# Optimization experiments

Hardware: AMD Instinct MI355X
Metric: run time of the kernel (lower is better)

## Reference

```python
import jax, jax.numpy as jnp
import numpy as np
from jax import lax

DIM = 1024
INNER = 2048  # dim * expand_factor
STATE = 64
B, T = 4, 2048
DECAY = 0.95
INPUT_FACTOR = 0.05
LN_EPS = 1e-5


def setup_inputs() -> dict:
    key = jax.random.key(0)
    ks = jax.random.split(key, 8)
    s = 0.02  # small weight scale
    return {
        "x": jax.random.normal(ks[0], (B, T, DIM), jnp.float32),
        "W_in": jax.random.normal(ks[1], (2 * INNER, DIM), jnp.float32) * s,
        "conv_w": jax.random.normal(ks[2], (INNER, 1, 4), jnp.float32) * s,
        "conv_b": jax.random.normal(ks[3], (INNER,), jnp.float32) * s,
        "W_B": jax.random.normal(ks[4], (STATE, INNER), jnp.float32) * s,
        "W_C": jax.random.normal(ks[5], (INNER, STATE), jnp.float32) * s,
        "D_param": jax.random.normal(ks[6], (INNER,), jnp.float32) * s,
        "W_out": jax.random.normal(ks[7], (DIM, INNER), jnp.float32) * s,
        "ln_gamma": jnp.ones((DIM,), jnp.float32),
        "ln_beta": jnp.zeros((DIM,), jnp.float32),
    }


def _layernorm(x, g, b):
    mu = jnp.mean(x, axis=-1, keepdims=True)
    var = jnp.mean(jnp.square(x - mu), axis=-1, keepdims=True)
    return (x - mu) * lax.rsqrt(var + LN_EPS) * g + b


def reference(x, W_in, conv_w, conv_b, W_B, W_C, D_param, W_out, ln_gamma, ln_beta):
    Bn, Tn, Dn = x.shape
    # in_proj -> split into input/gate halves
    x_proj = jnp.einsum("btd,ed->bte", x, W_in)  # [B,T,2*INNER]
    x_input, x_gate = jnp.split(x_proj, 2, axis=-1)
    # depthwise causal conv1d (torch pad=3 then slice [:T] == left-pad 3)
    xc = lax.conv_general_dilated(
        x_input.transpose(0, 2, 1),  # [B,C,T]
        conv_w,                       # [C,1,4]
        window_strides=(1,),
        padding=[(3, 0)],
        feature_group_count=INNER,
    ) + conv_b[None, :, None]
    u = jax.nn.silu(xc).transpose(0, 2, 1)  # [B,T,INNER]
    # linear recurrence: h_t = 0.95*h_{t-1} + 0.05*B_proj(u_t); h_0 = 0
    Bu = jnp.einsum("btc,sc->bts", u, W_B)  # [B,T,STATE]

    def step(h, bu_t):
        h = DECAY * h + INPUT_FACTOR * bu_t
        return h, h

    h0 = jnp.zeros((Bn, STATE), x.dtype)
    _, hs = lax.scan(step, h0, Bu.transpose(1, 0, 2))  # hs: [T,B,STATE]
    hs = hs.transpose(1, 0, 2)  # [B,T,STATE]
    y = jnp.einsum("bts,cs->btc", hs, W_C) + D_param * u  # [B,T,INNER]
    y = y * jax.nn.silu(x_gate)
    y = jnp.einsum("btc,dc->btd", y, W_out)  # [B,T,DIM]
    return _layernorm(y + x, ln_gamma, ln_beta)
```

## Files before the change

### kernel.cpp

```cpp
#include <hip/hip_runtime.h>
#include <hip/hip_bf16.h>

#define T_SEQ 2048
#define DIMD  1024
#define INNER 2048
#define STATE 64
#define BATCH 4
#define NCHUNK 64
#define CHUNK_L (T_SEQ / NCHUNK)
#define MROWS (BATCH * T_SEQ)
#define PSTRIDE ((long)MROWS * STATE)

typedef __hip_bfloat16 bf16;
typedef __attribute__((ext_vector_type(8))) short bf16x8v;
typedef __attribute__((ext_vector_type(4))) float f32x4v;
typedef __attribute__((ext_vector_type(4))) short short4v;

__device__ __forceinline__ float b2f(short s) {
    unsigned u = ((unsigned)(unsigned short)s) << 16;
    float f;
    __builtin_memcpy(&f, &u, 4);
    return f;
}
__device__ __forceinline__ short f2b(float f) {
    bf16 h = __float2bfloat16(f);
    short s;
    __builtin_memcpy(&s, &h, 2);
    return s;
}

__device__ __forceinline__ void gld_lds16(void* lds, const void* gsrc) {
    __builtin_amdgcn_global_load_lds(
        (const __attribute__((address_space(1))) unsigned*)gsrc,
        (__attribute__((address_space(3))) unsigned*)lds, 16, 0, 0);
}

template<int N> __device__ __forceinline__ void waitcnt_vm() {
    if constexpr (N == 16)      asm volatile("s_waitcnt vmcnt(16)" ::: "memory");
    else if constexpr (N == 8)  asm volatile("s_waitcnt vmcnt(8)" ::: "memory");
    else if constexpr (N == 6)  asm volatile("s_waitcnt vmcnt(6)" ::: "memory");
    else if constexpr (N == 4)  asm volatile("s_waitcnt vmcnt(4)" ::: "memory");
    else if constexpr (N == 2)  asm volatile("s_waitcnt vmcnt(2)" ::: "memory");
    else                        asm volatile("s_waitcnt vmcnt(0)" ::: "memory");
}
__device__ __forceinline__ void block_barrier() {
    asm volatile("" ::: "memory");
    __builtin_amdgcn_s_barrier();
    asm volatile("" ::: "memory");
}

template<int XSWZ>
__device__ __forceinline__ void swz_block(int& bx, int& by) {
    if constexpr (XSWZ == 1) {
        const int gx = gridDim.x;
        const int nwg = gx * gridDim.y;
        int id = by * gx + bx;
        const int cpx = nwg >> 3;
        id = (id & 7) * cpx + (id >> 3);
        bx = id % gx; by = id / gx;
    } else if constexpr (XSWZ == 2) {
        const int gx = gridDim.x;
        const int gy = gridDim.y;
        const int id = by * gx + bx;
        const int xcd = id & 7;
        const int c   = id >> 3;
        const int rowsX = gy >> 3;
        const int rw  = gx >> 2;
        const int r   = c >> 4;
        const int pos = c & 15;
        const int rbx = (r % rw) << 2;
        const int rby = (r / rw) << 2;
        bx = rbx + (pos & 3);
        by = xcd * rowsX + rby + (pos >> 2);
    }
}

template<int EPI, int XSWZ>
__global__ __launch_bounds__(512, 2)
void gemm_8ph(const short* __restrict__ A, const short* __restrict__ B,
              void* __restrict__ Cout, int M, int N, int K)
{
    __shared__ __align__(16) short As[2][2][128 * 64];
    __shared__ __align__(16) short Bs[2][2][128 * 64];

    int bx = blockIdx.x, by = blockIdx.y;
    swz_block<XSWZ>(bx, by);

    const int tid  = threadIdx.x;
    const int lane = tid & 63;
    const int wave = tid >> 6;
    const int wm2 = (wave >> 2) & 1;
    const int wn2 = wave & 3;
    const long bm = (long)by * 256;
    const long bn = (long)bx * 256;

    const int rsel = lane & 15;
    const int ssrc = (((tid & 7) ^ ((tid >> 3) & 7)) * 8);
    const int swz  = lane & 7;

    f32x4v acc[4][4][2];
#pragma unroll
    for (int q = 0; q < 4; q++)
#pragma unroll
        for (int m = 0; m < 4; m++)
#pragma unroll
            for (int n = 0; n < 2; n++)
                acc[q][m][n] = (f32x4v){0.f, 0.f, 0.f, 0.f};

    const int nt = K / 64;

    auto stage_half = [&](int tt, int h) {
        const int buf = tt & 1;
        const int half = h >> 1;
        const int k0 = tt * 64;
#pragma unroll
        for (int i = 0; i < 2; i++) {
            const int j = i * 512 + tid;
            if (h & 1)
                gld_lds16(&Bs[buf][half][j * 8],
                          &B[(bn + half * 128 + (j >> 3)) * (long)K + k0 + ssrc]);
            else
                gld_lds16(&As[buf][half][j * 8],
                          &A[(bm + half * 128 + (j >> 3)) * (long)K + k0 + ssrc]);
        }
    };

    stage_half(0, 0); stage_half(0, 1); stage_half(0, 2); stage_half(0, 3);

    for (int t = 0; t < nt; ++t) {
        const int buf = t & 1;
        const bool pf = (t + 1 < nt);
#pragma unroll
        for (int h = 0; h < 4; ++h) {
            if (pf) {
                if (h == 0) waitcnt_vm<4>();
                else if (h == 1) waitcnt_vm<4>();
                else if (h == 2) waitcnt_vm<4>();
            } else {
                if (h == 0) waitcnt_vm<4>();
                else if (h == 1) waitcnt_vm<2>();
                else if (h == 2) waitcnt_vm<0>();
            }
            block_barrier();

            const int QM[4] = {0, 1, 1, 0};
            const int QN[4] = {0, 0, 1, 1};
            const int qm = QM[h], qn = QN[h];
            bf16x8v af[4][2], bfv[2][2];
#pragma unroll
            for (int kkh = 0; kkh < 2; kkh++) {
                const int slog = kkh * 4 + (lane >> 4);
                const int soff = ((slog ^ swz) * 8);
#pragma unroll
                for (int m = 0; m < 4; m++) {
                    const int ar = wm2 * 64 + m * 16 + rsel;
                    af[m][kkh] = *(const bf16x8v*)&As[buf][qm][ar * 64 + soff];
                }
#pragma unroll
                for (int n = 0; n < 2; n++) {
                    const int br = wn2 * 32 + n * 16 + rsel;
                    bfv[n][kkh] = *(const bf16x8v*)&Bs[buf][qn][br * 64 + soff];
                }
            }
            if (pf) stage_half(t + 1, h);

            asm volatile("s_waitcnt lgkmcnt(0)" ::: "memory");
            __builtin_amdgcn_sched_barrier(0);
            __builtin_amdgcn_s_setprio(1);
#pragma unroll
            for (int kkh = 0; kkh < 2; kkh++)
#pragma unroll
                for (int m = 0; m < 4; m++)
#pragma unroll
                    for (int n = 0; n < 2; n++)
                        acc[h][m][n] = __builtin_amdgcn_mfma_f32_16x16x32_bf16(
                            af[m][kkh], bfv[n][kkh], acc[h][m][n], 0, 0, 0);
            __builtin_amdgcn_s_setprio(0);
        }
    }

#pragma unroll
    for (int q = 0; q < 4; q++) {
        const int QM[4] = {0, 1, 1, 0};
        const int QN[4] = {0, 0, 1, 1};
#pragma unroll
        for (int m = 0; m < 4; m++) {
#pragma unroll
            for (int n = 0; n < 2; n++) {
                const long col  = bn + QN[q] * 128 + wn2 * 32 + n * 16 + (lane & 15);
                const long row0 = bm + QM[q] * 128 + wm2 * 64 + m * 16 + (lane >> 4) * 4;
#pragma unroll
                for (int j = 0; j < 4; j++) {
                    const long idx = (row0 + j) * (long)N + col;
                    ((short*)Cout)[idx] = f2b(acc[q][m][n][j]);
                }
            }
        }
    }
}

template<int BM, int BN, int BK, int WR, int WC, int EPI, int SPLITK, int XSWZ>
__global__ __launch_bounds__(WR*WC*64, 2)
void gemm_ring(const short* __restrict__ A, const short* __restrict__ B,
               void* __restrict__ Cout, int M, int N, int K,
               const short* __restrict__ u_ptr, const short* __restrict__ gate_ptr,
               const float* __restrict__ Dp)
{
    constexpr int MFR = BM / (WR * 16);
    constexpr int NFR = BN / (WC * 16);
    constexpr int THREADS = WR * WC * 64;
    constexpr int UPR = BK / 8;
    constexpr int AISS = (BM * UPR) / THREADS;
    constexpr int BISS = (BN * UPR) / THREADS;
    constexpr int LPS  = AISS + BISS;
    __shared__ __align__(16) short As[2][BM * BK];
    __shared__ __align__(16) short Bs[2][BN * BK];

    int bx = blockIdx.x, by = blockIdx.y;
    swz_block<XSWZ>(bx, by);

    const int tid  = threadIdx.x;
    const int lane = tid & 63;
    const int wave = tid >> 6;
    const int wm = (wave / WC) * (MFR * 16);
    const int wn = (wave % WC) * (NFR * 16);
    const long bm = (long)by * BM;
    const long bn = (long)bx * BN;

    f32x4v acc[MFR][NFR];
#pragma unroll
    for (int m = 0; m < MFR; m++)
#pragma unroll
        for (int n = 0; n < NFR; n++)
            acc[m][n] = (f32x4v){0.f, 0.f, 0.f, 0.f};

    const int rsel = lane & 15;
    const int ssrc = (((tid & 7) ^ ((tid >> 3) & 7)) * 8);
    const int swz  = lane & 7;

    int kbeg = 0, kend = K;
    if constexpr (SPLITK > 1) {
        const int kch = K / SPLITK;
        kbeg = blockIdx.z * kch;
        kend = kbeg + kch;
    }
    const int nt = (kend - kbeg) / BK;

    auto stage = [&](int buf, int k0) {
#pragma unroll
        for (int i = 0; i < AISS; i++) {
            const int j = i * THREADS + tid;
            gld_lds16(&As[buf][j * 8],
                      &A[(bm + (j >> 3)) * (long)K + k0 + ssrc]);
        }
#pragma unroll
        for (int i = 0; i < BISS; i++) {
            const int j = i * THREADS + tid;
            gld_lds16(&Bs[buf][j * 8],
                      &B[(bn + (j >> 3)) * (long)K + k0 + ssrc]);
        }
    };
    auto compute = [&](int buf) {
#pragma unroll
        for (int kk = 0; kk < BK; kk += 32) {
            const int slog = (kk >> 3) + (lane >> 4);
            const int soff = ((slog ^ swz) * 8);
            bf16x8v af[MFR], bfv[NFR];
#pragma unroll
            for (int m = 0; m < MFR; m++)
                af[m] = *(const bf16x8v*)&As[buf][(wm + m * 16 + rsel) * BK + soff];
#pragma unroll
            for (int n = 0; n < NFR; n++)
                bfv[n] = *(const bf16x8v*)&Bs[buf][(wn + n * 16 + rsel) * BK + soff];
#pragma unroll
            for (int m = 0; m < MFR; m++)
#pragma unroll
                for (int n = 0; n < NFR; n++)
                    acc[m][n] = __builtin_amdgcn_mfma_f32_16x16x32_bf16(
                        af[m], bfv[n], acc[m][n], 0, 0, 0);
        }
    };

    stage(0, kbeg);
    for (int t = 0; t < nt; ++t) {
        const bool pf = (t + 1 < nt);
        if (pf) stage((t + 1) & 1, kbeg + (t + 1) * BK);
        if (pf) waitcnt_vm<LPS>();
        else    waitcnt_vm<0>();
        block_barrier();
        compute(t & 1);
        block_barrier();
    }

    float* fout = (float*)Cout;
    if constexpr (SPLITK > 1)
        fout += (long)blockIdx.z * (long)M * N;

#pragma unroll
    for (int m = 0; m < MFR; m++) {
#pragma unroll
        for (int n = 0; n < NFR; n++) {
            const long col  = bn + wn + n * 16 + (lane & 15);
            const long row0 = bm + wm + m * 16 + (lane >> 4) * 4;
#pragma unroll
            for (int j = 0; j < 4; j++) {
                const long row = row0 + j;
                const float v = acc[m][n][j];
                const long idx = row * (long)N + col;
                if constexpr (EPI == 0) {
                    ((short*)Cout)[idx] = f2b(v);
                } else if constexpr (EPI == 1) {
                    fout[idx] = v;
                } else if constexpr (EPI == 2) {
                    float uv = b2f(u_ptr[row * (long)INNER + col]);
                    float gv = b2f(gate_ptr[row * (long)(2 * INNER) + col]);
                    float yv = v + Dp[col] * uv;
                    float sg = gv / (1.f + __expf(-gv));
                    ((short*)Cout)[idx] = f2b(yv * sg);
                } else {
                    ((short*)Cout)[idx] = f2b(v + b2f(u_ptr[idx]));
                }
            }
        }
    }
}

__global__ __launch_bounds__(256)
void conv_silu_kernel(const short* __restrict__ xproj, const float* __restrict__ cw,
                      const float* __restrict__ cb, short* __restrict__ u)
{
    const int bt = blockIdx.x;
    const int t  = bt & (T_SEQ - 1);
    const int c0 = threadIdx.x * 8;

    float wreg[4][8];
#pragma unroll
    for (int i = 0; i < 8; i++) {
        float4 wv = *(const float4*)&cw[(c0 + i) * 4];
        wreg[0][i] = wv.x; wreg[1][i] = wv.y; wreg[2][i] = wv.z; wreg[3][i] = wv.w;
    }
    float acc[8];
#pragma unroll
    for (int i = 0; i < 8; i++) acc[i] = cb[c0 + i];

#pragma unroll
    for (int k = 0; k < 4; k++) {
        if (t - 3 + k < 0) continue;
        bf16x8v v = *(const bf16x8v*)&xproj[(long)(bt - 3 + k) * (2 * INNER) + c0];
#pragma unroll
        for (int i = 0; i < 8; i++) acc[i] += b2f(v[i]) * wreg[k][i];
    }
    short o[8];
#pragma unroll
    for (int i = 0; i < 8; i++) {
        float s = acc[i] / (1.f + __expf(-acc[i]));
        o[i] = f2b(s);
    }
    *(bf16x8v*)&u[(long)bt * INNER + c0] = *(const bf16x8v*)o;
}

__global__ __launch_bounds__(64)
void scan_local_kernel(const float* __restrict__ Bu, float* __restrict__ locfin)
{
    const int b  = blockIdx.x / NCHUNK;
    const int ch = blockIdx.x % NCHUNK;
    const long base = ((long)b * T_SEQ + (long)ch * CHUNK_L) * STATE + threadIdx.x;
    float h = 0.f;
#pragma unroll
    for (int t = 0; t < CHUNK_L; t++) {
        const long o = base + (long)t * STATE;
        float bu = (Bu[o] + Bu[o + PSTRIDE]) + (Bu[o + 2 * PSTRIDE] + Bu[o + 3 * PSTRIDE]);
        h = 0.95f * h + 0.05f * bu;
    }
    locfin[(long)blockIdx.x * STATE + threadIdx.x] = h;
}

__global__ __launch_bounds__(256)
void carry_kernel(const float* __restrict__ locfin, float* __restrict__ carry,
                  float decayL)
{
    __shared__ float sm[BATCH * NCHUNK * STATE];
    for (int i = threadIdx.x; i < BATCH * NCHUNK * STATE; i += 256)
        sm[i] = locfin[i];
    __syncthreads();
    const int b = threadIdx.x >> 6, s = threadIdx.x & 63;
    float c = 0.f;
    for (int ch = 0; ch < NCHUNK; ch++) {
        const int idx = (b * NCHUNK + ch) * STATE + s;
        carry[idx] = c;
        c = decayL * c + sm[idx];
    }
}

__global__ __launch_bounds__(64)
void scan_apply_kernel(const float* __restrict__ Bu, const float* __restrict__ carry,
                       short* __restrict__ hs)
{
    const int b  = blockIdx.x / NCHUNK;
    const int ch = blockIdx.x % NCHUNK;
    const long base = ((long)b * T_SEQ + (long)ch * CHUNK_L) * STATE + threadIdx.x;
    float h = carry[(long)blockIdx.x * STATE + threadIdx.x];
#pragma unroll
    for (int t = 0; t < CHUNK_L; t++) {
        const long o = base + (long)t * STATE;
        float bu = (Bu[o] + Bu[o + PSTRIDE]) + (Bu[o + 2 * PSTRIDE] + Bu[o + 3 * PSTRIDE]);
        h = 0.95f * h + 0.05f * bu;
        hs[o] = f2b(h);
    }
}

__global__ __launch_bounds__(256)
void ln_kernel(const short* __restrict__ yx, const float* __restrict__ g,
               const float* __restrict__ b, float* __restrict__ out)
{
    const int row = blockIdx.x;
    const int c   = threadIdx.x * 4;
    const long off = (long)row * DIMD + c;
    const short4v yv = *(const short4v*)&yx[off];
    float s0 = b2f(yv[0]), s1 = b2f(yv[1]), s2 = b2f(yv[2]), s3 = b2f(yv[3]);
    float sum = s0 + s1 + s2 + s3;
    float sq  = s0 * s0 + s1 * s1 + s2 * s2 + s3 * s3;
#pragma unroll
    for (int o = 32; o > 0; o >>= 1) {
        sum += __shfl_down(sum, o);
        sq  += __shfl_down(sq, o);
    }
    __shared__ float rs[4], rq[4];
    const int wave = threadIdx.x >> 6, lane = threadIdx.x & 63;
    if (lane == 0) { rs[wave] = sum; rq[wave] = sq; }
    __syncthreads();
    float tsum = rs[0] + rs[1] + rs[2] + rs[3];
    float tsq  = rq[0] + rq[1] + rq[2] + rq[3];
    float mu  = tsum * (1.f / DIMD);
    float inv = rsqrtf(tsq * (1.f / DIMD) - mu * mu + 1e-5f);
    float4 gv = *(const float4*)&g[c];
    float4 bv = *(const float4*)&b[c];
    float4 ov;
    ov.x = (s0 - mu) * inv * gv.x + bv.x;
    ov.y = (s1 - mu) * inv * gv.y + bv.y;
    ov.z = (s2 - mu) * inv * gv.z + bv.z;
    ov.w = (s3 - mu) * inv * gv.w + bv.w;
    *(float4*)&out[off] = ov;
}

#define C4_X   2097152L
#define C4_W1  (C4_X + 1048576L)
#define C4_WB  (C4_W1 + 32768L)
#define C4_WC  (C4_WB + 32768L)
#define C4_TOT (C4_WC + 524288L)

__global__ __launch_bounds__(256)
void cvt5_kernel(const float* __restrict__ x, const float* __restrict__ w1,
                 const float* __restrict__ wB, const float* __restrict__ wC,
                 const float* __restrict__ wO, short* __restrict__ dst)
{
    const long i = (long)blockIdx.x * 256 + threadIdx.x;
    if (i >= C4_TOT) return;
    const float* s;
    long off;
    if      (i < C4_X)  { s = x;  off = i; }
    else if (i < C4_W1) { s = w1; off = i - C4_X; }
    else if (i < C4_WB) { s = wB; off = i - C4_W1; }
    else if (i < C4_WC) { s = wC; off = i - C4_WB; }
    else                { s = wO; off = i - C4_WC; }
    float4 v = *(const float4*)&s[off * 4];
    short4v o = { f2b(v.x), f2b(v.y), f2b(v.z), f2b(v.w) };
    *(short4v*)&dst[i * 4] = o;
}

extern "C" void kernel_launch(void* const* d_in, const int* in_sizes, int n_in,
                              void* d_out, int out_size, void* d_ws, size_t ws_size,
                              hipStream_t stream)
{
    const float* x     = (const float*)d_in[0];
    const float* W_in  = (const float*)d_in[1];
    const float* cw    = (const float*)d_in[2];
    const float* cb    = (const float*)d_in[3];
    const float* W_B   = (const float*)d_in[4];
    const float* W_C   = (const float*)d_in[5];
    const float* Dp    = (const float*)d_in[6];
    const float* W_out = (const float*)d_in[7];
    const float* ln_g  = (const float*)d_in[8];
    const float* ln_b  = (const float*)d_in[9];

    char* p = (char*)d_ws;
    short* xw    = (short*)(p);
    short* w1    = (short*)(p +  16777216);
    short* wB    = (short*)(p +  25165824);
    short* wC    = (short*)(p +  25427968);
    short* wO    = (short*)(p +  25690112);
    short* xproj = (short*)(p +  29884416);
    short* u     = (short*)(p +  96993280);
    short* hs    = (short*)(p + 132644864);
    short* yg    = u;
    short* yx    = xproj;
    float* BuP    = (float*)(p + 16777216);
    float* locfin = (float*)(p + 25165824);
    float* carry  = (float*)(p + 25231360);

    const int M = MROWS;

    cvt5_kernel<<<(int)((C4_TOT + 255) / 256), 256, 0, stream>>>(
        x, W_in, W_B, W_C, W_out, xw);

    gemm_8ph<0, 2><<<dim3(2 * INNER / 256, M / 256), 512, 0, stream>>>(
        xw, w1, xproj, M, 2 * INNER, DIMD);

    conv_silu_kernel<<<M, 256, 0, stream>>>(xproj, cw, cb, u);

    gemm_ring<64, 64, 64, 2, 2, 1, 4, 0><<<dim3(1, M / 64, 4), 256, 0, stream>>>(
        u, wB, BuP, M, STATE, INNER, nullptr, nullptr, nullptr);

    float decayL;
    {
        double dd = 1.0;
        for (int i = 0; i < CHUNK_L; i++) dd *= 0.95;
        decayL = (float)dd;
    }
    scan_local_kernel<<<BATCH * NCHUNK, STATE, 0, stream>>>(BuP, locfin);
    carry_kernel<<<1, 256, 0, stream>>>(locfin, carry, decayL);
    scan_apply_kernel<<<BATCH * NCHUNK, STATE, 0, stream>>>(BuP, carry, hs);

    gemm_ring<128, 128, 64, 2, 2, 2, 1, 1><<<dim3(INNER / 128, M / 128), 256, 0, stream>>>(
        hs, wC, yg, M, INNER, STATE, u, xproj + INNER, Dp);

    gemm_ring<256, 128, 64, 4, 2, 3, 1, 2><<<dim3(DIMD / 128, M / 256), 512, 0, stream>>>(
        yg, wO, yx, M, DIMD, INNER, xw, nullptr, nullptr);

    ln_kernel<<<M, 256, 0, stream>>>(yx, ln_g, ln_b, (float*)d_out);
}
```

Measured before the change: 247.6 us.

## Add dedicated C-projection GEMM with LDS-staged vectorized gating epilogue; retile out-proj

Replaces the generic ring GEMM for the hs·W_C projection with a single-K-tile kernel. It loads the full K=64 slice once, stages the accumulators through shared memory, and then runs the D·u skip and SiLU gate epilogue with 16-byte vector loads and stores instead of scattered scalar accesses. The epilogue reads u from the output buffer and overwrites it in place, so it relies on u and yg sharing storage. The output-projection GEMM is also retiled from 256x128 with 512 threads to 128x128 with 256 threads, which doubles the block count at the cost of less reuse per block.

Measured after the change: 242.8 us. About the same (-1.9%).

```diff
diff --git a/kernel.cpp b/kernel.cpp
--- a/kernel.cpp
+++ b/kernel.cpp
@@ -311,16 +311,114 @@
                     ((short*)Cout)[idx] = f2b(v);
                 } else if constexpr (EPI == 1) {
                     fout[idx] = v;
-                } else if constexpr (EPI == 2) {
-                    float uv = b2f(u_ptr[row * (long)INNER + col]);
-                    float gv = b2f(gate_ptr[row * (long)(2 * INNER) + col]);
-                    float yv = v + Dp[col] * uv;
-                    float sg = gv / (1.f + __expf(-gv));
-                    ((short*)Cout)[idx] = f2b(yv * sg);
                 } else {
                     ((short*)Cout)[idx] = f2b(v + b2f(u_ptr[idx]));
                 }
             }
+        }
+    }
+}
+
+#define EBS 132
+__global__ __launch_bounds__(256, 2)
+void gemm3_fused(const short* __restrict__ hs, const short* __restrict__ Wc,
+                 short* __restrict__ yg, const short* __restrict__ gate_ptr,
+                 const float* __restrict__ Dp)
+{
+    __shared__ __align__(16) short As[128 * 64];
+    __shared__ __align__(16) short Bs[128 * 64];
+    __shared__ __align__(16) float eb[64 * EBS];
+
+    const int tid  = threadIdx.x;
+    const int lane = tid & 63;
+    const int wave = tid >> 6;
+    const int wm = (wave >> 1) * 64;
+    const int wn = (wave & 1) * 64;
+    const long bm = (long)blockIdx.y * 128;
+    const long bn = (long)blockIdx.x * 128;
+
+    const int rsel = lane & 15;
+    const int ssrc = (((tid & 7) ^ ((tid >> 3) & 7)) * 8);
+    const int swz  = lane & 7;
+
+#pragma unroll
+    for (int i = 0; i < 4; i++) {
+        const int j = i * 256 + tid;
+        gld_lds16(&As[j * 8], &hs[(bm + (j >> 3)) * (long)STATE + ssrc]);
+    }
+#pragma unroll
+    for (int i = 0; i < 4; i++) {
+        const int j = i * 256 + tid;
+        gld_lds16(&Bs[j * 8], &Wc[(bn + (j >> 3)) * (long)STATE + ssrc]);
+    }
+    waitcnt_vm<0>();
+    block_barrier();
+
+    f32x4v acc[4][4];
+#pragma unroll
+    for (int m = 0; m < 4; m++)
+#pragma unroll
+        for (int n = 0; n < 4; n++)
+            acc[m][n] = (f32x4v){0.f, 0.f, 0.f, 0.f};
+
+#pragma unroll
+    for (int kk = 0; kk < 64; kk += 32) {
+        const int slog = (kk >> 3) + (lane >> 4);
+        const int soff = ((slog ^ swz) * 8);
+        bf16x8v af[4], bfv[4];
+#pragma unroll
+        for (int m = 0; m < 4; m++)
+            af[m] = *(const bf16x8v*)&As[(wm + m * 16 + rsel) * 64 + soff];
+#pragma unroll
+        for (int n = 0; n < 4; n++)
+            bfv[n] = *(const bf16x8v*)&Bs[(wn + n * 16 + rsel) * 64 + soff];
+#pragma unroll
+        for (int m = 0; m < 4; m++)
+#pragma unroll
+            for (int n = 0; n < 4; n++)
+                acc[m][n] = __builtin_amdgcn_mfma_f32_16x16x32_bf16(
+                    af[m], bfv[n], acc[m][n], 0, 0, 0);
+    }
+
+#pragma unroll
+    for (int p = 0; p < 2; p++) {
+        block_barrier();
+        if ((wm >> 6) == p) {
+#pragma unroll
+            for (int m = 0; m < 4; m++) {
+#pragma unroll
+                for (int n = 0; n < 4; n++) {
+                    const int cl = wn + n * 16 + (lane & 15);
+#pragma unroll
+                    for (int j = 0; j < 4; j++) {
+                        const int rl = m * 16 + (lane >> 4) * 4 + j;
+                        eb[rl * EBS + cl] = acc[m][n][j];
+                    }
+                }
+            }
+        }
+        block_barrier();
+#pragma unroll
+        for (int k = 0; k < 4; k++) {
+            const int unit = k * 256 + tid;
+            const int rl = unit >> 4, cg = (unit & 15) * 8;
+            const long grow = bm + p * 64 + rl;
+            const long gcol = bn + cg;
+            f32x4v y0 = *(const f32x4v*)&eb[rl * EBS + cg];
+            f32x4v y1 = *(const f32x4v*)&eb[rl * EBS + cg + 4];
+            bf16x8v uv = *(const bf16x8v*)&yg[grow * (long)INNER + gcol];
+            bf16x8v gv = *(const bf16x8v*)&gate_ptr[grow * (long)(2 * INNER) + gcol];
+            short o[8];
+#pragma unroll
+            for (int i = 0; i < 8; i++) {
+                const float yy = (i < 4 ? y0[i] : y1[i - 4]);
+                const float uu = b2f(uv[i]);
+                const float gg = b2f(gv[i]);
+                const float yv = yy + Dp[gcol + i] * uu;
+                const float sg = gg / (1.f + __expf(-gg));
+                o[i] = f2b(yv * sg);
+            }
+            *(bf16x8v*)&yg[grow * (long)INNER + gcol] = *(const bf16x8v*)o;
         }
     }
 }
@@ -521,10 +619,10 @@
     carry_kernel<<<1, 256, 0, stream>>>(locfin, carry, decayL);
     scan_apply_kernel<<<BATCH * NCHUNK, STATE, 0, stream>>>(BuP, carry, hs);
 
-    gemm_ring<128, 128, 64, 2, 2, 2, 1, 1><<<dim3(INNER / 128, M / 128), 256, 0, stream>>>(
-        hs, wC, yg, M, INNER, STATE, u, xproj + INNER, Dp);
-
-    gemm_ring<256, 128, 64, 4, 2, 3, 1, 2><<<dim3(DIMD / 128, M / 256), 512, 0, stream>>>(
+    gemm3_fused<<<dim3(INNER / 128, M / 128), 256, 0, stream>>>(
+        hs, wC, yg, xproj + INNER, Dp);
+
+    gemm_ring<128, 128, 64, 2, 2, 3, 1, 1><<<dim3(DIMD / 128, M / 128), 256, 0, stream>>>(
         yg, wO, yx, M, DIMD, INNER, xw, nullptr, nullptr);
 
     ln_kernel<<<M, 256, 0, stream>>>(yx, ln_g, ln_b, (float*)d_out);
```
